# Kernel tuning notes

Hardware: AMD Instinct MI355X
Metric: run time of the kernel (lower is better)

The kernel has to match this reference:

```python
import jax, jax.numpy as jnp
import numpy as np

K, D, B = 2048, 50257, 256
N_CLASS = 2

def setup_inputs() -> dict:
    key = jax.random.key(0)
    k1, k2, k3 = jax.random.split(key, 3)
    # strictly positive (probability-like) entries so log() is finite
    queue_anchor = jax.random.uniform(k1, (K, D), dtype=jnp.float32, minval=1e-3, maxval=1.0)
    query = jax.random.uniform(k2, (B, D), dtype=jnp.float32, minval=1e-3, maxval=1.0)
    queue_label = jax.random.randint(k3, (K,), 0, N_CLASS, dtype=jnp.int64)
    return {"query": query, "queue_anchor": queue_anchor, "queue_label": queue_label}

def reference(query, queue_anchor, queue_label):
    # torch code: mean_d( a[:,None,:] * (log a[:,None,:] - log q) ).T  -> [B, K]
    # algebraically identical, avoiding the (K,B,D) intermediate:
    #   kl[b,k] = mean_d(a_k * log a_k) - (1/D) * sum_d a_k[d] * log q_b[d]
    d = queue_anchor.shape[1]
    self_term = jnp.mean(queue_anchor * jnp.log(queue_anchor), axis=1)        # [K]
    cross_term = jnp.einsum('kd,bd->kb', queue_anchor, jnp.log(query)) / d    # [K, B]
    kl_distance = (self_term[:, None] - cross_term).T                          # [B, K]
    # knn == 1 path: nearest anchor's label per query
    return queue_label[jnp.argmin(kl_distance, axis=1)]                        # [B]
```

## Files before the change

### kernel.cpp

```cpp
#include <hip/hip_runtime.h>


constexpr int K   = 2048;
constexpr int D   = 50257;
constexpr int B   = 256;
constexpr int BM  = 128;
constexpr int BN  = 128;
constexpr int BKD = 64;
constexpr int SCH = 24;
constexpr int DP  = 50320;

typedef __attribute__((ext_vector_type(8))) short bf16x8;
typedef __attribute__((ext_vector_type(4))) float f32x4;
typedef __attribute__((ext_vector_type(8))) unsigned short u16x8;

__device__ inline unsigned short f2bf_rne(float f) {
    union { float f; unsigned u; } v; v.f = f;
    unsigned r = v.u + 0x7FFFu + ((v.u >> 16) & 1u);
    return (unsigned short)(r >> 16);
}

__global__ __launch_bounds__(256)
void lq_kernel(const float* __restrict__ q, unsigned short* __restrict__ lq)
{
    const int stride = gridDim.x * blockDim.x;
    const int total  = B * (DP / 4);
    for (int c = blockIdx.x * blockDim.x + threadIdx.x; c < total; c += stride) {
        const int b   = c / (DP / 4);
        const int off = (c % (DP / 4)) * 4;
        ushort4 w;
        float v0 = (off + 0 < D) ? __logf(q[(size_t)b * D + off + 0]) : 0.f;
        float v1 = (off + 1 < D) ? __logf(q[(size_t)b * D + off + 1]) : 0.f;
        float v2 = (off + 2 < D) ? __logf(q[(size_t)b * D + off + 2]) : 0.f;
        float v3 = (off + 3 < D) ? __logf(q[(size_t)b * D + off + 3]) : 0.f;
        w.x = f2bf_rne(v0); w.y = f2bf_rne(v1); w.z = f2bf_rne(v2); w.w = f2bf_rne(v3);
        *reinterpret_cast<ushort4*>(&lq[(size_t)b * DP + off]) = w;
    }
}

template<bool USELQ>
__global__ __launch_bounds__(512, 4)
void gemm_kernel(const float* __restrict__ query,
                 const float* __restrict__ anchor,
                 const unsigned short* __restrict__ lq,
                 float* __restrict__ cross,
                 float* __restrict__ selftot,
                 int dc)
{
    const int t    = threadIdx.x;
    const int k0   = blockIdx.x * BM;
    const int b0   = blockIdx.y * BN;
    const int d0   = blockIdx.z * dc;
    const int dend = min(d0 + dc, D);
    if (d0 >= dend) return;

    __shared__ __align__(16) unsigned short Al[BM * 64];
    __shared__ __align__(16) unsigned short Ql[BN * 64];

    const int trow = t >> 2;
    const int tq   = t & 3;
    const int sw8  = (trow & 7) << 3;

    const float*          Arow  = anchor + (size_t)(k0 + trow) * D;
    const float*          Qrow  = query  + (size_t)(b0 + trow) * D;
    const unsigned short* LQrow = lq     + (size_t)(b0 + trow) * DP;

    const int w    = t >> 6;
    const int lane = t & 63;
    const int wm   = (w >> 2) * 64;
    const int wn   = (w & 3) * 32;
    const int lrow = lane & 15;
    const int kg   = lane >> 4;

    f32x4 acc[4][2];
#pragma unroll
    for (int mt = 0; mt < 4; ++mt)
#pragma unroll
        for (int nt = 0; nt < 2; ++nt)
#pragma unroll
            for (int i = 0; i < 4; ++i) acc[mt][nt][i] = 0.f;

    float selfacc = 0.f;
    const bool doself = (blockIdx.y == 0);

    float areg[16];
    u16x8 qreg[2];
    float qf32[16];

    auto load_step = [&](int dt) {
        const int dbase = dt + tq * 16;
#pragma unroll
        for (int jj = 0; jj < 16; ++jj) {
            const int d = dbase + jj;
            areg[jj] = (d < dend) ? Arow[d] : 0.f;
        }
        if constexpr (USELQ) {
            qreg[0] = *reinterpret_cast<const u16x8*>(&LQrow[dbase]);
            qreg[1] = *reinterpret_cast<const u16x8*>(&LQrow[dbase + 8]);
        } else {
#pragma unroll
            for (int jj = 0; jj < 16; ++jj) {
                const int d = dbase + jj;
                qf32[jj] = (d < dend) ? Qrow[d] : 1.f;
            }
        }
    };

    load_step(d0);

    for (int dt = d0; dt < dend; dt += BKD) {
        unsigned short abf[16];
#pragma unroll
        for (int jj = 0; jj < 16; ++jj) abf[jj] = f2bf_rne(areg[jj]);
        if (doself) {
#pragma unroll
            for (int jj = 0; jj < 16; ++jj)
                if (areg[jj] > 0.f) selfacc = fmaf(areg[jj], __logf(areg[jj]), selfacc);
        }
        u16x8 qb0, qb1;
        if constexpr (USELQ) {
            qb0 = qreg[0]; qb1 = qreg[1];
        } else {
#pragma unroll
            for (int j = 0; j < 8; ++j) qb0[j] = f2bf_rne(__logf(qf32[j]));
#pragma unroll
            for (int j = 0; j < 8; ++j) qb1[j] = f2bf_rne(__logf(qf32[8 + j]));
        }

        __syncthreads();
        {
            unsigned short* a0 = &Al[trow * 64 + ((tq * 16)     ^ sw8)];
            unsigned short* a1 = &Al[trow * 64 + ((tq * 16 + 8) ^ sw8)];
            reinterpret_cast<ushort4*>(a0)[0] = ushort4{abf[0], abf[1], abf[2],  abf[3]};
            reinterpret_cast<ushort4*>(a0)[1] = ushort4{abf[4], abf[5], abf[6],  abf[7]};
            reinterpret_cast<ushort4*>(a1)[0] = ushort4{abf[8], abf[9], abf[10], abf[11]};
            reinterpret_cast<ushort4*>(a1)[1] = ushort4{abf[12], abf[13], abf[14], abf[15]};
            *reinterpret_cast<u16x8*>(&Ql[trow * 64 + ((tq * 16)     ^ sw8)]) = qb0;
            *reinterpret_cast<u16x8*>(&Ql[trow * 64 + ((tq * 16 + 8) ^ sw8)]) = qb1;
        }
        __syncthreads();

        if (dt + BKD < dend) load_step(dt + BKD);

#pragma unroll
        for (int half = 0; half < 2; ++half) {
            const int dd = half * 32;
            bf16x8 af[4], qf[2];
#pragma unroll
            for (int mt = 0; mt < 4; ++mt) {
                const int r = wm + mt * 16 + lrow;
                const int c = (dd + kg * 8) ^ ((r & 7) << 3);
                af[mt] = *reinterpret_cast<const bf16x8*>(&Al[r * 64 + c]);
            }
#pragma unroll
            for (int nt = 0; nt < 2; ++nt) {
                const int r = wn + nt * 16 + lrow;
                const int c = (dd + kg * 8) ^ ((r & 7) << 3);
                qf[nt] = *reinterpret_cast<const bf16x8*>(&Ql[r * 64 + c]);
            }
#pragma unroll
            for (int mt = 0; mt < 4; ++mt)
#pragma unroll
                for (int nt = 0; nt < 2; ++nt)
                    acc[mt][nt] = __builtin_amdgcn_mfma_f32_16x16x32_bf16(
                        af[mt], qf[nt], acc[mt][nt], 0, 0, 0);
        }
    }

#pragma unroll
    for (int mt = 0; mt < 4; ++mt)
#pragma unroll
        for (int nt = 0; nt < 2; ++nt) {
            const int kb = k0 + wm + mt * 16 + kg * 4;
            const int bb = b0 + wn + nt * 16 + lrow;
            float* dst = &cross[(size_t)bb * K + kb];
#pragma unroll
            for (int i = 0; i < 4; ++i) atomicAdd(&dst[i], acc[mt][nt][i]);
        }
    if (doself) {
        float s = selfacc;
        s += __shfl_xor(s, 1);
        s += __shfl_xor(s, 2);
        if (tq == 0) atomicAdd(&selftot[k0 + trow], s);
    }
}

__global__ __launch_bounds__(256)
void topk_kernel(const float* __restrict__ cross, const float* __restrict__ selftot,
                 int* __restrict__ cand)
{
    const int b = blockIdx.x, t = threadIdx.x;
    float v[8];
#pragma unroll
    for (int i = 0; i < 8; ++i) {
        const int k = i * 256 + t;
        v[i] = selftot[k] - cross[(size_t)b * K + k];
    }
    __shared__ float sv[256];
    __shared__ int   si[256];
    for (int r = 0; r < 8; ++r) {
        float bv = 3.4e38f; int bk = K;
#pragma unroll
        for (int i = 0; i < 8; ++i) {
            const int k = i * 256 + t;
            if (v[i] < bv) { bv = v[i]; bk = k; }
        }
        sv[t] = bv; si[t] = bk;
        __syncthreads();
        for (int off = 128; off > 0; off >>= 1) {
            if (t < off) {
                if (sv[t + off] < sv[t] || (sv[t + off] == sv[t] && si[t + off] < si[t])) {
                    sv[t] = sv[t + off]; si[t] = si[t + off];
                }
            }
            __syncthreads();
        }
        const int kwin = si[0];
        if ((kwin & 255) == t) v[kwin >> 8] = 3.4e38f;
        if (t == 0) cand[b * 8 + r] = kwin;
        __syncthreads();
    }
}

__global__ __launch_bounds__(256)
void rescore_kernel(const float* __restrict__ query, const float* __restrict__ anchor,
                    const float* __restrict__ selftot, const int* __restrict__ cand,
                    const int* __restrict__ label, int* __restrict__ out)
{
    const int b = blockIdx.x, t = threadIdx.x;
    int ks[8];
#pragma unroll
    for (int c = 0; c < 8; ++c) ks[c] = cand[b * 8 + c];
    const float* qrow = query + (size_t)b * D;

    double acc[8];
#pragma unroll
    for (int c = 0; c < 8; ++c) acc[c] = 0.0;

    for (int d = t; d < D; d += 256) {
        const double lqv = (double)logf(qrow[d]);
#pragma unroll
        for (int c = 0; c < 8; ++c)
            acc[c] = fma((double)anchor[(size_t)ks[c] * D + d], lqv, acc[c]);
    }

    __shared__ double red[256];
    __shared__ double fin[8];
    for (int c = 0; c < 8; ++c) {
        red[t] = acc[c];
        __syncthreads();
        for (int off = 128; off > 0; off >>= 1) {
            if (t < off) red[t] += red[t + off];
            __syncthreads();
        }
        if (t == 0) fin[c] = red[0];
        __syncthreads();
    }

    if (t == 0) {
        float best = 3.4e38f; int bk = K;
#pragma unroll
        for (int c = 0; c < 8; ++c) {
            const float sc = selftot[ks[c]] - (float)fin[c];
            if (sc < best || (sc == best && ks[c] < bk)) { best = sc; bk = ks[c]; }
        }
        out[b] = label[bk];
    }
}

extern "C" void kernel_launch(void* const* d_in, const int* in_sizes, int n_in,
                              void* d_out, int out_size, void* d_ws, size_t ws_size,
                              hipStream_t stream)
{
    const float* query  = (const float*)d_in[0];
    const float* anchor = (const float*)d_in[1];
    const int*   label  = (const int*)d_in[2];
    int* out = (int*)d_out;

    float* cross   = (float*)d_ws;
    float* selftot = cross + (size_t)B * K;
    int*   cand    = (int*)(selftot + K);
    unsigned short* lq = (unsigned short*)(cand + B * 8);

    const size_t need_lq = ((size_t)B * K + K + B * 8) * 4 + (size_t)B * DP * 2;
    const bool uselq = (ws_size >= need_lq);

    const int dc = (((D + SCH - 1) / SCH) + BKD - 1) / BKD * BKD;

    hipMemsetAsync(cross, 0, ((size_t)B * K + K) * sizeof(float), stream);
    if (uselq) {
        lq_kernel<<<1024, 256, 0, stream>>>(query, lq);
        gemm_kernel<true><<<dim3(K / BM, B / BN, SCH), 512, 0, stream>>>(
            query, anchor, lq, cross, selftot, dc);
    } else {
        gemm_kernel<false><<<dim3(K / BM, B / BN, SCH), 512, 0, stream>>>(
            query, anchor, lq, cross, selftot, dc);
    }
    topk_kernel<<<B, 256, 0, stream>>>(cross, selftot, cand);
    rescore_kernel<<<B, 256, 0, stream>>>(query, anchor, selftot, cand, label, out);
}
```

Before: 641.7 us.

## Retile GEMM to cover the full batch, write split-K partials without atomics

The GEMM tile changes to 64 anchors by the full 256-query batch, so each anchor element is read and converted exactly once. Previously the anchor was read once per query tile and only the first tile computed the self term. Split-K partial products go to a workspace buffer with plain vector stores instead of atomics. The self-term partials are reduced in a separate kernel, and topk sums the partials itself. Other changes: anchor loads use aligned float4 reads with a phase shift, the rescore candidates drop from 8 to 4, and rescore is split over two D halves with a final combine kernel. The cost is a large partial buffer (32×256×2048 floats) that topk must re-read, plus extra launches.

```diff
diff --git a/kernel.cpp b/kernel.cpp
--- a/kernel.cpp
+++ b/kernel.cpp
@@ -4,11 +4,12 @@
 constexpr int K   = 2048;
 constexpr int D   = 50257;
 constexpr int B   = 256;
-constexpr int BM  = 128;
-constexpr int BN  = 128;
-constexpr int BKD = 64;
-constexpr int SCH = 24;
+constexpr int BM  = 64;
+constexpr int BN  = 256;
+constexpr int BK  = 64;
+constexpr int SCH = 32;
 constexpr int DP  = 50320;
+constexpr int NC  = 4;
 
 typedef __attribute__((ext_vector_type(8))) short bf16x8;
 typedef __attribute__((ext_vector_type(4))) float f32x4;
@@ -38,167 +39,187 @@
     }
 }
 
-template<bool USELQ>
+template<bool WSP>
 __global__ __launch_bounds__(512, 4)
-void gemm_kernel(const float* __restrict__ query,
-                 const float* __restrict__ anchor,
+void gemm_kernel(const float* __restrict__ anchor,
                  const unsigned short* __restrict__ lq,
-                 float* __restrict__ cross,
-                 float* __restrict__ selftot,
+                 float* __restrict__ outc,
+                 float* __restrict__ selfp,
                  int dc)
 {
     const int t    = threadIdx.x;
     const int k0   = blockIdx.x * BM;
-    const int b0   = blockIdx.y * BN;
-    const int d0   = blockIdx.z * dc;
+    const int z    = blockIdx.y;
+    const int d0   = z * dc;
     const int dend = min(d0 + dc, D);
-    if (d0 >= dend) return;
 
     __shared__ __align__(16) unsigned short Al[BM * 64];
     __shared__ __align__(16) unsigned short Ql[BN * 64];
 
-    const int trow = t >> 2;
-    const int tq   = t & 3;
-    const int sw8  = (trow & 7) << 3;
-
-    const float*          Arow  = anchor + (size_t)(k0 + trow) * D;
-    const float*          Qrow  = query  + (size_t)(b0 + trow) * D;
-    const unsigned short* LQrow = lq     + (size_t)(b0 + trow) * DP;
+    const int rowA = t >> 3;
+    const int tq8  = t & 7;
+    const int ar   = k0 + rowA;
+    const int swA  = (rowA & 7) << 3;
+    const float* Arow = anchor + (size_t)ar * D;
+
+    const int rowQ = t >> 1;
+    const int hq   = t & 1;
+    const int swQ  = (rowQ & 7) << 3;
+    const unsigned short* LQrow = lq + (size_t)rowQ * DP;
 
     const int w    = t >> 6;
     const int lane = t & 63;
-    const int wm   = (w >> 2) * 64;
-    const int wn   = (w & 3) * 32;
+    const int wm   = (w >> 2) * 32;
+    const int wn   = (w & 3) * 64;
     const int lrow = lane & 15;
     const int kg   = lane >> 4;
 
-    f32x4 acc[4][2];
-#pragma unroll
-    for (int mt = 0; mt < 4; ++mt)
-#pragma unroll
-        for (int nt = 0; nt < 2; ++nt)
+    f32x4 acc[2][4];
+#pragma unroll
+    for (int mt = 0; mt < 2; ++mt)
+#pragma unroll
+        for (int nt = 0; nt < 4; ++nt)
 #pragma unroll
             for (int i = 0; i < 4; ++i) acc[mt][nt][i] = 0.f;
 
     float selfacc = 0.f;
-    const bool doself = (blockIdx.y == 0);
-
-    float areg[16];
-    u16x8 qreg[2];
-    float qf32[16];
+
+    float wf[12];
+    int   ph = 0;
+    u16x8 qreg[4];
 
     auto load_step = [&](int dt) {
-        const int dbase = dt + tq * 16;
-#pragma unroll
-        for (int jj = 0; jj < 16; ++jj) {
-            const int d = dbase + jj;
-            areg[jj] = (d < dend) ? Arow[d] : 0.f;
-        }
-        if constexpr (USELQ) {
-            qreg[0] = *reinterpret_cast<const u16x8*>(&LQrow[dbase]);
-            qreg[1] = *reinterpret_cast<const u16x8*>(&LQrow[dbase + 8]);
+        const int dbase = dt + tq8 * 8;
+        if (dbase + 12 <= dend) {
+            const size_t g0 = (size_t)ar * D + dbase;
+            ph = (int)(g0 & 3);
+            const float4* wp = reinterpret_cast<const float4*>(anchor + (g0 - ph));
+            const float4 w0 = wp[0], w1 = wp[1], w2 = wp[2];
+            wf[0] = w0.x; wf[1]  = w0.y; wf[2]  = w0.z; wf[3]  = w0.w;
+            wf[4] = w1.x; wf[5]  = w1.y; wf[6]  = w1.z; wf[7]  = w1.w;
+            wf[8] = w2.x; wf[9]  = w2.y; wf[10] = w2.z; wf[11] = w2.w;
         } else {
-#pragma unroll
-            for (int jj = 0; jj < 16; ++jj) {
-                const int d = dbase + jj;
-                qf32[jj] = (d < dend) ? Qrow[d] : 1.f;
-            }
-        }
+            ph = 0;
+#pragma unroll
+            for (int j = 0; j < 8; ++j) {
+                const int d = dbase + j;
+                wf[j] = (d < dend) ? Arow[d] : 0.f;
+            }
+#pragma unroll
+            for (int j = 8; j < 12; ++j) wf[j] = 0.f;
+        }
+        const int qb = dt + hq * 32;
+#pragma unroll
+        for (int g = 0; g < 4; ++g)
+            qreg[g] = *reinterpret_cast<const u16x8*>(&LQrow[qb + 8 * g]);
     };
 
     load_step(d0);
 
-    for (int dt = d0; dt < dend; dt += BKD) {
-        unsigned short abf[16];
-#pragma unroll
-        for (int jj = 0; jj < 16; ++jj) abf[jj] = f2bf_rne(areg[jj]);
-        if (doself) {
-#pragma unroll
-            for (int jj = 0; jj < 16; ++jj)
-                if (areg[jj] > 0.f) selfacc = fmaf(areg[jj], __logf(areg[jj]), selfacc);
-        }
-        u16x8 qb0, qb1;
-        if constexpr (USELQ) {
-            qb0 = qreg[0]; qb1 = qreg[1];
-        } else {
-#pragma unroll
-            for (int j = 0; j < 8; ++j) qb0[j] = f2bf_rne(__logf(qf32[j]));
-#pragma unroll
-            for (int j = 0; j < 8; ++j) qb1[j] = f2bf_rne(__logf(qf32[8 + j]));
+    for (int dt = d0; dt < dend; dt += BK) {
+        float s1[9], av[8];
+#pragma unroll
+        for (int j = 0; j < 9; ++j) s1[j] = (ph & 2) ? wf[j + 2] : wf[j];
+#pragma unroll
+        for (int j = 0; j < 8; ++j) av[j] = (ph & 1) ? s1[j + 1] : s1[j];
+
+        unsigned short abf[8];
+#pragma unroll
+        for (int j = 0; j < 8; ++j) {
+            if (av[j] > 0.f) selfacc = fmaf(av[j], __logf(av[j]), selfacc);
+            abf[j] = f2bf_rne(av[j]);
         }
 
         __syncthreads();
         {
-            unsigned short* a0 = &Al[trow * 64 + ((tq * 16)     ^ sw8)];
-            unsigned short* a1 = &Al[trow * 64 + ((tq * 16 + 8) ^ sw8)];
-            reinterpret_cast<ushort4*>(a0)[0] = ushort4{abf[0], abf[1], abf[2],  abf[3]};
-            reinterpret_cast<ushort4*>(a0)[1] = ushort4{abf[4], abf[5], abf[6],  abf[7]};
-            reinterpret_cast<ushort4*>(a1)[0] = ushort4{abf[8], abf[9], abf[10], abf[11]};
-            reinterpret_cast<ushort4*>(a1)[1] = ushort4{abf[12], abf[13], abf[14], abf[15]};
-            *reinterpret_cast<u16x8*>(&Ql[trow * 64 + ((tq * 16)     ^ sw8)]) = qb0;
-            *reinterpret_cast<u16x8*>(&Ql[trow * 64 + ((tq * 16 + 8) ^ sw8)]) = qb1;
-        }
-        __syncthreads();
-
-        if (dt + BKD < dend) load_step(dt + BKD);
+            unsigned short* a0 = &Al[rowA * 64 + ((tq8 * 8) ^ swA)];
+            reinterpret_cast<ushort4*>(a0)[0] = ushort4{abf[0], abf[1], abf[2], abf[3]};
+            reinterpret_cast<ushort4*>(a0)[1] = ushort4{abf[4], abf[5], abf[6], abf[7]};
+#pragma unroll
+            for (int g = 0; g < 4; ++g)
+                *reinterpret_cast<u16x8*>(&Ql[rowQ * 64 + ((hq * 32 + 8 * g) ^ swQ)]) = qreg[g];
+        }
+        __syncthreads();
+
+        if (dt + BK < dend) load_step(dt + BK);
 
 #pragma unroll
         for (int half = 0; half < 2; ++half) {
             const int dd = half * 32;
-            bf16x8 af[4], qf[2];
-#pragma unroll
-            for (int mt = 0; mt < 4; ++mt) {
+            bf16x8 af[2], qf[4];
+#pragma unroll
+            for (int mt = 0; mt < 2; ++mt) {
                 const int r = wm + mt * 16 + lrow;
                 const int c = (dd + kg * 8) ^ ((r & 7) << 3);
                 af[mt] = *reinterpret_cast<const bf16x8*>(&Al[r * 64 + c]);
             }
 #pragma unroll
-            for (int nt = 0; nt < 2; ++nt) {
+            for (int nt = 0; nt < 4; ++nt) {
                 const int r = wn + nt * 16 + lrow;
                 const int c = (dd + kg * 8) ^ ((r & 7) << 3);
                 qf[nt] = *reinterpret_cast<const bf16x8*>(&Ql[r * 64 + c]);
             }
 #pragma unroll
-            for (int mt = 0; mt < 4; ++mt)
-#pragma unroll
-                for (int nt = 0; nt < 2; ++nt)
+            for (int mt = 0; mt < 2; ++mt)
+#pragma unroll
+                for (int nt = 0; nt < 4; ++nt)
                     acc[mt][nt] = __builtin_amdgcn_mfma_f32_16x16x32_bf16(
                         af[mt], qf[nt], acc[mt][nt], 0, 0, 0);
         }
     }
 
 #pragma unroll
-    for (int mt = 0; mt < 4; ++mt)
-#pragma unroll
-        for (int nt = 0; nt < 2; ++nt) {
-            const int kb = k0 + wm + mt * 16 + kg * 4;
-            const int bb = b0 + wn + nt * 16 + lrow;
-            float* dst = &cross[(size_t)bb * K + kb];
-#pragma unroll
-            for (int i = 0; i < 4; ++i) atomicAdd(&dst[i], acc[mt][nt][i]);
-        }
-    if (doself) {
-        float s = selfacc;
-        s += __shfl_xor(s, 1);
-        s += __shfl_xor(s, 2);
-        if (tq == 0) atomicAdd(&selftot[k0 + trow], s);
-    }
+    for (int mt = 0; mt < 2; ++mt)
+#pragma unroll
+        for (int nt = 0; nt < 4; ++nt) {
+            const int kk = k0 + wm + mt * 16 + kg * 4;
+            const int bb = wn + nt * 16 + lrow;
+            if (WSP) {
+                *reinterpret_cast<f32x4*>(&outc[((size_t)z * B + bb) * K + kk]) = acc[mt][nt];
+            } else {
+                float* dst = &outc[(size_t)bb * K + kk];
+#pragma unroll
+                for (int i = 0; i < 4; ++i) atomicAdd(&dst[i], acc[mt][nt][i]);
+            }
+        }
+
+    float s = selfacc;
+    s += __shfl_xor(s, 1);
+    s += __shfl_xor(s, 2);
+    s += __shfl_xor(s, 4);
+    if (tq8 == 0) selfp[(size_t)z * K + ar] = s;
 }
 
 __global__ __launch_bounds__(256)
-void topk_kernel(const float* __restrict__ cross, const float* __restrict__ selftot,
-                 int* __restrict__ cand)
+void selfsum_kernel(const float* __restrict__ selfp, float* __restrict__ selftot, int sch)
+{
+    const int k = blockIdx.x * 256 + threadIdx.x;
+    float s = 0.f;
+    for (int z = 0; z < sch; ++z) s += selfp[(size_t)z * K + k];
+    selftot[k] = s;
+}
+
+template<bool WSP>
+__global__ __launch_bounds__(256)
+void topk_kernel(const float* __restrict__ outc, const float* __restrict__ selftot,
+                 int* __restrict__ cand, int sch)
 {
     const int b = blockIdx.x, t = threadIdx.x;
     float v[8];
 #pragma unroll
     for (int i = 0; i < 8; ++i) {
         const int k = i * 256 + t;
-        v[i] = selftot[k] - cross[(size_t)b * K + k];
+        float cv = 0.f;
+        if (WSP) {
+            for (int z = 0; z < sch; ++z) cv += outc[((size_t)z * B + b) * K + k];
+        } else {
+            cv = outc[(size_t)b * K + k];
+        }
+        v[i] = selftot[k] - cv;
     }
     __shared__ float sv[256];
     __shared__ int   si[256];
-    for (int r = 0; r < 8; ++r) {
+    for (int r = 0; r < NC; ++r) {
         float bv = 3.4e38f; int bk = K;
 #pragma unroll
         for (int i = 0; i < 8; ++i) {
@@ -217,55 +238,62 @@
         }
         const int kwin = si[0];
         if ((kwin & 255) == t) v[kwin >> 8] = 3.4e38f;
-        if (t == 0) cand[b * 8 + r] = kwin;
-        __syncthreads();
-    }
-}
-
-__global__ __launch_bounds__(256)
+        if (t == 0) cand[b * NC + r] = kwin;
+        __syncthreads();
+    }
+}
+
+__global__ __launch_bounds__(512)
 void rescore_kernel(const float* __restrict__ query, const float* __restrict__ anchor,
-                    const float* __restrict__ selftot, const int* __restrict__ cand,
-                    const int* __restrict__ label, int* __restrict__ out)
-{
-    const int b = blockIdx.x, t = threadIdx.x;
-    int ks[8];
-#pragma unroll
-    for (int c = 0; c < 8; ++c) ks[c] = cand[b * 8 + c];
+                    const int* __restrict__ cand, double* __restrict__ pp)
+{
+    const int b = blockIdx.x, h = blockIdx.y, t = threadIdx.x;
+    const int dlo = h * 25129;
+    const int dhi = min(D, dlo + 25129);
+    int ks[NC];
+#pragma unroll
+    for (int c = 0; c < NC; ++c) ks[c] = cand[b * NC + c];
     const float* qrow = query + (size_t)b * D;
 
-    double acc[8];
-#pragma unroll
-    for (int c = 0; c < 8; ++c) acc[c] = 0.0;
-
-    for (int d = t; d < D; d += 256) {
+    double a4[NC];
+#pragma unroll
+    for (int c = 0; c < NC; ++c) a4[c] = 0.0;
+
+    for (int d = dlo + t; d < dhi; d += 512) {
         const double lqv = (double)logf(qrow[d]);
 #pragma unroll
-        for (int c = 0; c < 8; ++c)
-            acc[c] = fma((double)anchor[(size_t)ks[c] * D + d], lqv, acc[c]);
-    }
-
-    __shared__ double red[256];
-    __shared__ double fin[8];
-    for (int c = 0; c < 8; ++c) {
-        red[t] = acc[c];
-        __syncthreads();
-        for (int off = 128; off > 0; off >>= 1) {
+        for (int c = 0; c < NC; ++c)
+            a4[c] = fma((double)anchor[(size_t)ks[c] * D + d], lqv, a4[c]);
+    }
+
+    __shared__ double red[512];
+    for (int c = 0; c < NC; ++c) {
+        red[t] = a4[c];
+        __syncthreads();
+        for (int off = 256; off > 0; off >>= 1) {
             if (t < off) red[t] += red[t + off];
             __syncthreads();
         }
-        if (t == 0) fin[c] = red[0];
-        __syncthreads();
-    }
-
-    if (t == 0) {
-        float best = 3.4e38f; int bk = K;
-#pragma unroll
-        for (int c = 0; c < 8; ++c) {
-            const float sc = selftot[ks[c]] - (float)fin[c];
-            if (sc < best || (sc == best && ks[c] < bk)) { best = sc; bk = ks[c]; }
-        }
-        out[b] = label[bk];
-    }
+        if (t == 0) pp[((size_t)b * 2 + h) * NC + c] = red[0];
+        __syncthreads();
+    }
+}
+
+__global__ __launch_bounds__(256)
+void final_kernel(const double* __restrict__ pp, const float* __restrict__ selftot,
+                  const int* __restrict__ cand, const int* __restrict__ label,
+                  int* __restrict__ out)
+{
+    const int b = threadIdx.x;
+    float best = 3.4e38f; int bk = K;
+#pragma unroll
+    for (int c = 0; c < NC; ++c) {
+        const int k = cand[b * NC + c];
+        const double cv = pp[((size_t)b * 2 + 0) * NC + c] + pp[((size_t)b * 2 + 1) * NC + c];
+        const float sc = selftot[k] - (float)cv;
+        if (sc < best || (sc == best && k < bk)) { best = sc; bk = k; }
+    }
+    out[b] = label[bk];
 }
 
 extern "C" void kernel_launch(void* const* d_in, const int* in_sizes, int n_in,
@@ -277,25 +305,41 @@
     const int*   label  = (const int*)d_in[2];
     int* out = (int*)d_out;
 
-    float* cross   = (float*)d_ws;
-    float* selftot = cross + (size_t)B * K;
-    int*   cand    = (int*)(selftot + K);
-    unsigned short* lq = (unsigned short*)(cand + B * 8);
-
-    const size_t need_lq = ((size_t)B * K + K + B * 8) * 4 + (size_t)B * DP * 2;
-    const bool uselq = (ws_size >= need_lq);
-
-    const int dc = (((D + SCH - 1) / SCH) + BKD - 1) / BKD * BKD;
-
-    hipMemsetAsync(cross, 0, ((size_t)B * K + K) * sizeof(float), stream);
-    if (uselq) {
-        lq_kernel<<<1024, 256, 0, stream>>>(query, lq);
-        gemm_kernel<true><<<dim3(K / BM, B / BN, SCH), 512, 0, stream>>>(
-            query, anchor, lq, cross, selftot, dc);
+    size_t cur = 0;
+    auto alloc = [&](size_t bytes, size_t al) -> void* {
+        cur = (cur + al - 1) & ~(al - 1);
+        void* p = (char*)d_ws + cur;
+        cur += bytes;
+        return p;
+    };
+    unsigned short* lq      = (unsigned short*)alloc((size_t)B * DP * 2, 16);
+    float*          selfp   = (float*)alloc((size_t)SCH * K * 4, 16);
+    float*          selftot = (float*)alloc((size_t)K * 4, 16);
+    int*            cand    = (int*)alloc((size_t)B * NC * 4, 16);
+    double*         pp      = (double*)alloc((size_t)B * 2 * NC * 8, 16);
+    float*          cross   = (float*)alloc((size_t)B * K * 4, 16);
+    float*          part    = (float*)alloc((size_t)SCH * B * K * 4, 16);
+    const bool wsp = (cur <= ws_size);
+
+    const int dc = (((D + SCH - 1) / SCH) + BK - 1) / BK * BK;
+    const int sch_eff = (D + dc - 1) / dc;
+
+    lq_kernel<<<1024, 256, 0, stream>>>(query, lq);
+
+    if (wsp) {
+        gemm_kernel<true><<<dim3(K / BM, sch_eff), 512, 0, stream>>>(
+            anchor, lq, part, selfp, dc);
     } else {
-        gemm_kernel<false><<<dim3(K / BM, B / BN, SCH), 512, 0, stream>>>(
-            query, anchor, lq, cross, selftot, dc);
-    }
-    topk_kernel<<<B, 256, 0, stream>>>(cross, selftot, cand);
-    rescore_kernel<<<B, 256, 0, stream>>>(query, anchor, selftot, cand, label, out);
-}
+        hipMemsetAsync(cross, 0, (size_t)B * K * sizeof(float), stream);
+        gemm_kernel<false><<<dim3(K / BM, sch_eff), 512, 0, stream>>>(
+            anchor, lq, cross, selfp, dc);
+    }
+
+    selfsum_kernel<<<K / 256, 256, 0, stream>>>(selfp, selftot, sch_eff);
+
+    if (wsp) topk_kernel<true><<<B, 256, 0, stream>>>(part, selftot, cand, sch_eff);
+    else     topk_kernel<false><<<B, 256, 0, stream>>>(cross, selftot, cand, sch_eff);
+
+    rescore_kernel<<<dim3(B, 2), 512, 0, stream>>>(query, anchor, cand, pp);
+    final_kernel<<<1, 256, 0, stream>>>(pp, selftot, cand, label, out);
+}
```

After: 588.9 us. 8.2% less time.
